# Performance work log

Hardware: AMD Instinct MI355X
Metric: run time of the kernel (lower is better)

## Reference

```python
import jax, jax.numpy as jnp
import numpy as np

N_EMBED = 4096
N_Q_HEADS = 32
N_KV_HEADS = 8
HEAD_DIM = N_EMBED // N_Q_HEADS  # 128
N_GROUPS = N_Q_HEADS // N_KV_HEADS  # 4
ROPE_BASE = 10000.0
BATCH, SEQ = 1, 2048


def setup_inputs() -> dict:
    key = jax.random.key(0)
    ks = jax.random.split(key, 5)
    hidden_state = jax.random.normal(ks[0], (BATCH, SEQ, N_EMBED), dtype=jnp.float32)
    # additive causal mask: 0 on/below diagonal, -inf above (SDPA float-mask semantics)
    causal = jnp.tril(jnp.ones((SEQ, SEQ), dtype=bool))
    attention_mask = jnp.where(causal, 0.0, -jnp.inf).astype(jnp.float32)[None, None]
    position_ids = jnp.arange(SEQ, dtype=jnp.int32)[None, :].repeat(BATCH, axis=0)
    s = 0.02
    Wq = jax.random.normal(ks[1], (N_EMBED, N_EMBED), dtype=jnp.float32) * s
    Wk = jax.random.normal(ks[2], (N_KV_HEADS * HEAD_DIM, N_EMBED), dtype=jnp.float32) * s
    Wv = jax.random.normal(ks[3], (N_KV_HEADS * HEAD_DIM, N_EMBED), dtype=jnp.float32) * s
    Wo = jax.random.normal(ks[4], (N_EMBED, N_EMBED), dtype=jnp.float32) * s
    return {"hidden_state": hidden_state, "attention_mask": attention_mask,
            "position_ids": position_ids, "Wq": Wq, "Wk": Wk, "Wv": Wv, "Wo": Wo}


def _rope_tables(position_ids):
    # mimic torch: inv_freq built in fp16 then used as float
    exponent = (jnp.arange(0, HEAD_DIM, 2, dtype=jnp.float16) / HEAD_DIM)
    inv_freq = (1.0 / (ROPE_BASE ** exponent)).astype(jnp.float32)  # [hd/2]
    m = position_ids.astype(jnp.float32)  # [bs, seq]
    m_theta = m[:, :, None] * inv_freq[None, None, :]  # [bs, seq, hd/2]
    m_theta = jnp.concatenate([m_theta, m_theta], axis=-1)  # [bs, seq, hd]
    return jnp.cos(m_theta), jnp.sin(m_theta)


def _rotate_half(x):
    half = x.shape[-1] // 2
    return jnp.concatenate([-x[..., half:], x[..., :half]], axis=-1)


def reference(hidden_state, attention_mask, position_ids, Wq, Wk, Wv, Wo):
    bs, seq, _ = hidden_state.shape
    q = (hidden_state @ Wq.T).reshape(bs, seq, N_Q_HEADS, HEAD_DIM).transpose(0, 2, 1, 3)
    k = (hidden_state @ Wk.T).reshape(bs, seq, N_KV_HEADS, HEAD_DIM).transpose(0, 2, 1, 3)
    v = (hidden_state @ Wv.T).reshape(bs, seq, N_KV_HEADS, HEAD_DIM).transpose(0, 2, 1, 3)

    cos, sin = _rope_tables(position_ids)
    cos, sin = cos[:, None], sin[:, None]  # broadcast over heads
    q = q * cos + _rotate_half(q) * sin
    k = k * cos + _rotate_half(k) * sin

    # GQA: group query heads per KV head instead of materializing KV copies
    qg = q.reshape(bs, N_KV_HEADS, N_GROUPS, seq, HEAD_DIM)
    scale = 1.0 / jnp.sqrt(jnp.float32(HEAD_DIM))
    scores = jnp.einsum('bhgqd,bhkd->bhgqk', qg, k) * scale + attention_mask[:, :, None]
    probs = jax.nn.softmax(scores, axis=-1)
    attn = jnp.einsum('bhgqk,bhkd->bhgqd', probs, v)  # [bs, kvh, g, seq, hd]
    attn = attn.reshape(bs, N_Q_HEADS, seq, HEAD_DIM).transpose(0, 2, 1, 3).reshape(bs, seq, N_EMBED)
    return attn @ Wo.T
```

## Files before the change

### kernel.cpp

```cpp
#include <hip/hip_runtime.h>
#include <hip/hip_bf16.h>

#define SEQ 2048
#define LDQKV 6144

typedef __attribute__((ext_vector_type(8))) __bf16 bf16x8;
typedef __attribute__((ext_vector_type(4))) __bf16 bf16x4;
typedef __attribute__((ext_vector_type(4))) float f32x4;

__device__ __forceinline__ void gload_lds16(const void* g, void* l) {
  __builtin_amdgcn_global_load_lds((__attribute__((address_space(1))) void*)(g),
                                   (__attribute__((address_space(3))) void*)(l), 16, 0, 0);
}

struct CvtArgs {
  const float* src0; const float* src1; const float* src2; const float* src3; const float* src4;
  __bf16* dst0; __bf16* dst1; __bf16* dst2; __bf16* dst3; __bf16* dst4;
};
__global__ __launch_bounds__(256) void cvt_all(CvtArgs a) {
  int b = blockIdx.x;
  const float* s; __bf16* d; int boff;
  if (b < 4096)       { s = a.src0; d = a.dst0; boff = b; }
  else if (b < 12288) { s = a.src1; d = a.dst1; boff = b - 4096; }
  else if (b < 14336) { s = a.src2; d = a.dst2; boff = b - 12288; }
  else if (b < 16384) { s = a.src3; d = a.dst3; boff = b - 14336; }
  else                { s = a.src4; d = a.dst4; boff = b - 16384; }
  long i = ((long)boff * 256 + threadIdx.x) * 8;
  f32x4 v0 = *(const f32x4*)(s + i);
  f32x4 v1 = *(const f32x4*)(s + i + 4);
  bf16x8 o;
  #pragma unroll
  for (int j = 0; j < 4; ++j) { o[j] = (__bf16)v0[j]; o[j + 4] = (__bf16)v1[j]; }
  *(bf16x8*)(d + i) = o;
}

__global__ __launch_bounds__(256) void rope_tab_k(const int* __restrict__ pos,
                                                  float* __restrict__ tab) {
  int i = blockIdx.x * 256 + threadIdx.x;
  int s = i >> 6, j = i & 63;
  float p = (float)pos[s];
  float pw = powf(10000.0f, (float)j * (1.0f / 64.0f));
  _Float16 ph = (_Float16)pw;
  _Float16 ivh = (_Float16)(1.0f / (float)ph);
  float freq = (float)ivh;
  float th = p * freq;
  tab[i] = cosf(th);
  tab[SEQ * 64 + i] = sinf(th);
}

__global__ __launch_bounds__(256) void rope_apply_k(__bf16* __restrict__ qkv,
                                                    const float* __restrict__ tab) {
  int i = blockIdx.x * 256 + threadIdx.x;
  int dc = i & 7;
  int ht = (i >> 3) % 40;
  int s = i / 320;
  long col = (ht < 32) ? (long)ht * 128 : (long)4096 + (long)(ht - 32) * 128;
  __bf16* p = qkv + (long)s * LDQKV + col + dc * 8;
  bf16x8 lo = *(bf16x8*)p;
  bf16x8 hi = *(bf16x8*)(p + 64);
  const float* tc = tab + (long)s * 64 + dc * 8;
  const float* ts = tc + SEQ * 64;
  bf16x8 lo2, hi2;
  #pragma unroll
  for (int e = 0; e < 8; ++e) {
    float c = tc[e], sn = ts[e];
    float lv = (float)lo[e], hv = (float)hi[e];
    lo2[e] = (__bf16)(lv * c - hv * sn);
    hi2[e] = (__bf16)(hv * c + lv * sn);
  }
  *(bf16x8*)p = lo2;
  *(bf16x8*)(p + 64) = hi2;
}

template<int BN, int BUFS, bool OUT_BF16>
__global__ __launch_bounds__(512, 2) void gemmW(const __bf16* __restrict__ A,
                                                const __bf16* __restrict__ B,
                                                void* __restrict__ C,
                                                int K, int ldc) {
  constexpr int BHR = BN / 2;
  constexpr int NFR = BN / 128;
  constexpr int LB  = BHR / 64;
  constexpr int NA  = (BUFS == 3) ? 2 : 1;
  constexpr int TE  = (128 + BN) * 64;
  extern __shared__ __bf16 lds[];

  const int tid = threadIdx.x;
  const int wave = tid >> 6, lane = tid & 63;
  const int l15 = lane & 15, l4 = lane >> 4;
  const int wm = wave >> 2, wn = wave & 3;

  const int orig = blockIdx.x;
  const int swz = (orig & 7) * 32 + (orig >> 3);
  const int bx = swz & 15, by = swz >> 4;
  const long brow = (long)bx * 128, bcol = (long)by * BN;

  const int rS = tid >> 3;
  const int cS = ((tid & 7) * 8) ^ ((rS & 7) << 3);
  const int NT = K >> 6;

  auto bufp = [&](int b) -> __bf16* { return lds + b * TE; };
  auto stageA = [&](int b, int qm, int t) {
    gload_lds16(A + (brow + qm * 64 + rS) * (long)K + t * 64 + cS,
                bufp(b) + qm * 4096 + wave * 512);
  };
  auto stageB = [&](int b, int qn, int t) {
    #pragma unroll
    for (int i = 0; i < LB; ++i)
      gload_lds16(B + (bcol + qn * BHR + i * 64 + rS) * (long)K + t * 64 + cS,
                  bufp(b) + 8192 + qn * (BHR * 64) + i * 4096 + wave * 512);
  };

  bf16x8 afLo[2][2], afHi[2][2], b0[NFR][2], b1[NFR][2];
  auto readA = [&](bf16x8 (&dst)[2][2], int b, int qm) {
    #pragma unroll
    for (int mi = 0; mi < 2; ++mi) {
      int r = wm * 32 + mi * 16 + l15;
      #pragma unroll
      for (int kf = 0; kf < 2; ++kf) {
        int c = (kf * 32 + l4 * 8) ^ ((r & 7) << 3);
        dst[mi][kf] = *(const bf16x8*)&bufp(b)[qm * 4096 + r * 64 + c];
      }
    }
  };
  auto readB = [&](bf16x8 (&dst)[NFR][2], int b, int qn) {
    #pragma unroll
    for (int ni = 0; ni < NFR; ++ni) {
      int r = wn * (BN / 8) + ni * 16 + l15;
      #pragma unroll
      for (int kf = 0; kf < 2; ++kf) {
        int c = (kf * 32 + l4 * 8) ^ ((r & 7) << 3);
        dst[ni][kf] = *(const bf16x8*)&bufp(b)[8192 + qn * (BHR * 64) + r * 64 + c];
      }
    }
  };

  f32x4 acc[2][2][2][NFR] = {};
  auto mfmaQ = [&](bf16x8 (&af)[2][2], bf16x8 (&bf_)[NFR][2], f32x4 (&ac)[2][NFR]) {
    __builtin_amdgcn_s_setprio(1);
    #pragma unroll
    for (int mi = 0; mi < 2; ++mi)
      #pragma unroll
      for (int ni = 0; ni < NFR; ++ni)
        #pragma unroll
        for (int kf = 0; kf < 2; ++kf)
          ac[mi][ni] = __builtin_amdgcn_mfma_f32_16x16x32_bf16(af[mi][kf], bf_[ni][kf], ac[mi][ni], 0, 0, 0);
    __builtin_amdgcn_s_setprio(0);
  };

  #pragma unroll
  for (int tt = 0; tt < NA; ++tt) {
    stageA(tt % BUFS, 0, tt); stageB(tt % BUFS, 0, tt);
    stageA(tt % BUFS, 1, tt); stageB(tt % BUFS, 1, tt);
  }
  if constexpr (BUFS == 3) asm volatile("s_waitcnt vmcnt(6)" ::: "memory");
  else                     asm volatile("s_waitcnt vmcnt(0)" ::: "memory");
  __builtin_amdgcn_s_barrier();
  __builtin_amdgcn_sched_barrier(0);

  for (int t = 0; t < NT; ++t) {
    const int cur = t % BUFS, pre = (t + NA) % BUFS;
    const bool pf = (t + NA < NT);
    readA(afLo, cur, 0); readB(b0, cur, 0);
    if (pf) { stageA(pre, 0, t + NA); stageB(pre, 0, t + NA); }
    mfmaQ(afLo, b0, acc[0][0]);
    readA(afHi, cur, 1); readB(b1, cur, 1);
    if (pf) { stageA(pre, 1, t + NA); stageB(pre, 1, t + NA); }
    mfmaQ(afHi, b0, acc[1][0]);
    mfmaQ(afHi, b1, acc[1][1]);
    mfmaQ(afLo, b1, acc[0][1]);
    if (t + 1 < NT) {
      __builtin_amdgcn_sched_barrier(0);
      if constexpr (BUFS == 3) {
        if (pf) asm volatile("s_waitcnt vmcnt(6)" ::: "memory");
        else    asm volatile("s_waitcnt vmcnt(0)" ::: "memory");
      } else {
        asm volatile("s_waitcnt vmcnt(0)" ::: "memory");
      }
      __builtin_amdgcn_s_barrier();
      __builtin_amdgcn_sched_barrier(0);
    }
  }

  #pragma unroll
  for (int qm = 0; qm < 2; ++qm)
    #pragma unroll
    for (int qn = 0; qn < 2; ++qn)
      #pragma unroll
      for (int mi = 0; mi < 2; ++mi)
        #pragma unroll
        for (int ni = 0; ni < NFR; ++ni)
          #pragma unroll
          for (int j = 0; j < 4; ++j) {
            long rr = brow + qm * 64 + wm * 32 + mi * 16 + l4 * 4 + j;
            long cc = bcol + qn * BHR + wn * (BN / 8) + ni * 16 + l15;
            float v = acc[qm][qn][mi][ni][j];
            if (OUT_BF16) ((__bf16*)C)[rr * ldc + cc] = (__bf16)v;
            else          ((float*)C)[rr * ldc + cc] = v;
          }
}

__global__ __launch_bounds__(256) void flash_k(const __bf16* __restrict__ qkv,
                                               __bf16* __restrict__ ctx) {
  __shared__ __align__(16) __bf16 Kl[8192];
  __shared__ __align__(16) __bf16 Vt[8192];
  __shared__ __align__(16) __bf16 Pl[4][1024];

  const int bid = blockIdx.x;
  const int h = bid & 31;
  const int qt = 31 - (bid >> 5);
  const int kvh = h >> 2;
  const int q0 = qt * 64;
  const int tid = threadIdx.x, wave = tid >> 6, lane = tid & 63;
  const int l15 = lane & 15, l4 = lane >> 4;
  const int d2 = tid & 63, grp = tid >> 6;

  const __bf16* Qp = qkv + (long)h * 128;
  const __bf16* Kp = qkv + 4096 + (long)kvh * 128;
  const __bf16* Vp = qkv + 5120 + (long)kvh * 128;

  bf16x8 aq[4];
  {
    long qr = q0 + wave * 16 + l15;
    #pragma unroll
    for (int ks = 0; ks < 4; ++ks)
      aq[ks] = *(const bf16x8*)(Qp + qr * LDQKV + ks * 32 + l4 * 8);
  }
  f32x4 accO[8] = {};
  float lsum[4] = {0.f, 0.f, 0.f, 0.f};
  const float cexp = 0.08838834764831845f * 1.4426950408889634f;

  for (int kv0 = 0; kv0 <= q0; kv0 += 64) {
    __syncthreads();
    #pragma unroll
    for (int i = 0; i < 4; ++i) {
      int fo = i * 2048 + wave * 512 + lane * 8;
      int r = fo >> 7, c = fo & 127;
      int cs = c ^ ((r & 7) << 3);
      gload_lds16(Kp + (long)(kv0 + r) * LDQKV + cs, &Kl[i * 2048 + wave * 512]);
    }
    unsigned int vv[2][8];
    #pragma unroll
    for (int rep = 0; rep < 2; ++rep) {
      int cch = grp * 2 + rep;
      #pragma unroll
      for (int i = 0; i < 8; ++i)
        vv[rep][i] = *(const unsigned int*)(Vp + (long)(kv0 + cch * 8 + i) * LDQKV + 2 * d2);
    }
    #pragma unroll
    for (int rep = 0; rep < 2; ++rep) {
      int cch = grp * 2 + rep;
      #pragma unroll
      for (int half = 0; half < 2; ++half) {
        bf16x8 w;
        #pragma unroll
        for (int i = 0; i < 8; ++i)
          w[i] = __builtin_bit_cast(__bf16, (unsigned short)(vv[rep][i] >> (16 * half)));
        int d = 2 * d2 + half;
        *(bf16x8*)&Vt[d * 64 + ((cch * 8) ^ ((d2 & 7) * 8))] = w;
      }
    }
    __syncthreads();

    f32x4 s[4];
    #pragma unroll
    for (int t = 0; t < 4; ++t) s[t] = f32x4{0.f, 0.f, 0.f, 0.f};
    __builtin_amdgcn_s_setprio(1);
    #pragma unroll
    for (int t = 0; t < 4; ++t) {
      int r = t * 16 + l15;
      #pragma unroll
      for (int ks = 0; ks < 4; ++ks) {
        bf16x8 bk = *(const bf16x8*)&Kl[r * 128 + ((ks * 32 + l4 * 8) ^ ((r & 7) << 3))];
        s[t] = __builtin_amdgcn_mfma_f32_16x16x32_bf16(aq[ks], bk, s[t], 0, 0, 0);
      }
    }
    __builtin_amdgcn_s_setprio(0);

    const bool lastStep = (kv0 == q0);
    float pout[4][4];
    #pragma unroll
    for (int t = 0; t < 4; ++t)
      #pragma unroll
      for (int j = 0; j < 4; ++j) {
        float p = exp2f(s[t][j] * cexp);
        if (lastStep) {
          int qg = wave * 16 + l4 * 4 + j;
          int kg = t * 16 + l15;
          if (kg > qg) p = 0.f;
        }
        pout[t][j] = p;
      }
    #pragma unroll
    for (int j = 0; j < 4; ++j)
      lsum[j] += (pout[0][j] + pout[1][j]) + (pout[2][j] + pout[3][j]);

    #pragma unroll
    for (int t = 0; t < 4; ++t)
      #pragma unroll
      for (int j = 0; j < 4; ++j) {
        int r = l4 * 4 + j;
        int c = t * 16 + l15;
        Pl[wave][r * 64 + (c ^ ((r & 7) << 3))] = (__bf16)pout[t][j];
      }
    asm volatile("s_waitcnt lgkmcnt(0)" ::: "memory");
    __builtin_amdgcn_sched_barrier(0);
    bf16x8 ap[2];
    #pragma unroll
    for (int ks2 = 0; ks2 < 2; ++ks2) {
      int c = ks2 * 32 + l4 * 8;
      ap[ks2] = *(const bf16x8*)&Pl[wave][l15 * 64 + (c ^ ((l15 & 7) << 3))];
    }
    __builtin_amdgcn_s_setprio(1);
    #pragma unroll
    for (int dt = 0; dt < 8; ++dt) {
      int d = dt * 16 + l15;
      #pragma unroll
      for (int ks2 = 0; ks2 < 2; ++ks2) {
        int c = (ks2 * 32 + l4 * 8) ^ (((l15 >> 1) & 7) * 8);
        bf16x8 bv = *(const bf16x8*)&Vt[d * 64 + c];
        accO[dt] = __builtin_amdgcn_mfma_f32_16x16x32_bf16(ap[ks2], bv, accO[dt], 0, 0, 0);
      }
    }
    __builtin_amdgcn_s_setprio(0);
  }
  float rls[4];
  #pragma unroll
  for (int j = 0; j < 4; ++j) {
    float ls = lsum[j];
    ls += __shfl_xor(ls, 1, 16);
    ls += __shfl_xor(ls, 2, 16);
    ls += __shfl_xor(ls, 4, 16);
    ls += __shfl_xor(ls, 8, 16);
    rls[j] = 1.f / ls;
  }
  #pragma unroll
  for (int dt = 0; dt < 8; ++dt)
    #pragma unroll
    for (int j = 0; j < 4; ++j) {
      long qr = q0 + wave * 16 + l4 * 4 + j;
      long cc = (long)h * 128 + dt * 16 + l15;
      ctx[qr * 4096 + cc] = (__bf16)(accO[dt][j] * rls[j]);
    }
}

extern "C" void kernel_launch(void* const* d_in, const int* in_sizes, int n_in,
                              void* d_out, int out_size, void* d_ws, size_t ws_size,
                              hipStream_t stream) {
  const float* hs  = (const float*)d_in[0];
  const int*   pos = (const int*)d_in[2];
  const float* Wq  = (const float*)d_in[3];
  const float* Wk  = (const float*)d_in[4];
  const float* Wv  = (const float*)d_in[5];
  const float* Wo  = (const float*)d_in[6];
  char* ws = (char*)d_ws;
  __bf16* hsb  = (__bf16*)(ws + 0L);
  __bf16* wqkv = (__bf16*)(ws + 16777216L);
  __bf16* wob  = (__bf16*)(ws + 67108864L);
  __bf16* qkvb = (__bf16*)(ws + 100663296L);
  float*  tab  = (float*)(ws + 125829120L);
  __bf16* ctx  = (__bf16*)(ws + 126877696L);

  (void)hipFuncSetAttribute(reinterpret_cast<const void*>(&gemmW<384, 2, true>),
                            hipFuncAttributeMaxDynamicSharedMemorySize, 131072);
  (void)hipFuncSetAttribute(reinterpret_cast<const void*>(&gemmW<256, 3, false>),
                            hipFuncAttributeMaxDynamicSharedMemorySize, 147456);

  CvtArgs ca;
  ca.src0 = hs;  ca.dst0 = hsb;
  ca.src1 = Wq;  ca.dst1 = wqkv;
  ca.src2 = Wk;  ca.dst2 = wqkv + 16777216L;
  ca.src3 = Wv;  ca.dst3 = wqkv + 20971520L;
  ca.src4 = Wo;  ca.dst4 = wob;
  cvt_all<<<24576, 256, 0, stream>>>(ca);
  rope_tab_k<<<512, 256, 0, stream>>>(pos, tab);

  gemmW<384, 2, true><<<256, 512, 131072, stream>>>(hsb, wqkv, qkvb, 4096, 6144);

  rope_apply_k<<<2560, 256, 0, stream>>>(qkvb, tab);

  flash_k<<<1024, 256, 0, stream>>>(qkvb, ctx);

  gemmW<256, 3, false><<<256, 512, 147456, stream>>>(ctx, wob, d_out, 4096, 4096);
}
```

Measured before the change: 283.1 us.

## Interleave per-quarter staging with MFMA phases in double-buffered GEMM loop

For the two-buffer GEMM configuration, the main loop is restructured into four phases per k-tile. Each phase issues one quarter-tile global-to-LDS stage for the next tile, runs one MFMA quadrant, then waits on a partial vmcnt and a barrier. The goal is to spread memory traffic across the compute so loads overlap MFMA work, instead of staging everything up front and doing a full vmcnt(0) wait at the end. The cost is more barriers per iteration, and the vmcnt(4) counts only stay correct if each stage call issues the number of loads they assume.

```diff
diff --git a/kernel.cpp b/kernel.cpp
--- a/kernel.cpp
+++ b/kernel.cpp
@@ -147,37 +147,64 @@
     __builtin_amdgcn_s_setprio(0);
   };
 
-  #pragma unroll
-  for (int tt = 0; tt < NA; ++tt) {
-    stageA(tt % BUFS, 0, tt); stageB(tt % BUFS, 0, tt);
-    stageA(tt % BUFS, 1, tt); stageB(tt % BUFS, 1, tt);
-  }
-  if constexpr (BUFS == 3) asm volatile("s_waitcnt vmcnt(6)" ::: "memory");
-  else                     asm volatile("s_waitcnt vmcnt(0)" ::: "memory");
-  __builtin_amdgcn_s_barrier();
-  __builtin_amdgcn_sched_barrier(0);
-
-  for (int t = 0; t < NT; ++t) {
-    const int cur = t % BUFS, pre = (t + NA) % BUFS;
-    const bool pf = (t + NA < NT);
-    readA(afLo, cur, 0); readB(b0, cur, 0);
-    if (pf) { stageA(pre, 0, t + NA); stageB(pre, 0, t + NA); }
-    mfmaQ(afLo, b0, acc[0][0]);
-    readA(afHi, cur, 1); readB(b1, cur, 1);
-    if (pf) { stageA(pre, 1, t + NA); stageB(pre, 1, t + NA); }
-    mfmaQ(afHi, b0, acc[1][0]);
-    mfmaQ(afHi, b1, acc[1][1]);
-    mfmaQ(afLo, b1, acc[0][1]);
-    if (t + 1 < NT) {
-      __builtin_amdgcn_sched_barrier(0);
-      if constexpr (BUFS == 3) {
+  if constexpr (BUFS == 2) {
+    #define VM_WAIT4() asm volatile("s_waitcnt vmcnt(4)" ::: "memory")
+    #define PH_BAR()   do { __builtin_amdgcn_s_barrier(); __builtin_amdgcn_sched_barrier(0); } while (0)
+    stageA(0, 0, 0); stageB(0, 0, 0); stageA(0, 1, 0); stageB(0, 1, 0);
+    VM_WAIT4();
+    PH_BAR();
+    for (int t = 0; t < NT; ++t) {
+      const int buf = t & 1, nb = buf ^ 1;
+      const bool pf = (t + 1 < NT);
+      if (pf) stageA(nb, 0, t + 1);
+      readA(afLo, buf, 0); readB(b0, buf, 0);
+      mfmaQ(afLo, b0, acc[0][0]);
+      VM_WAIT4();
+      PH_BAR();
+      if (pf) stageB(nb, 0, t + 1);
+      readA(afHi, buf, 1);
+      mfmaQ(afHi, b0, acc[1][0]);
+      VM_WAIT4();
+      PH_BAR();
+      if (pf) stageA(nb, 1, t + 1);
+      readB(b1, buf, 1);
+      mfmaQ(afHi, b1, acc[1][1]);
+      PH_BAR();
+      if (pf) stageB(nb, 1, t + 1);
+      mfmaQ(afLo, b1, acc[0][1]);
+      VM_WAIT4();
+      PH_BAR();
+    }
+    #undef VM_WAIT4
+    #undef PH_BAR
+  } else {
+    #pragma unroll
+    for (int tt = 0; tt < NA; ++tt) {
+      stageA(tt % BUFS, 0, tt); stageB(tt % BUFS, 0, tt);
+      stageA(tt % BUFS, 1, tt); stageB(tt % BUFS, 1, tt);
+    }
+    asm volatile("s_waitcnt vmcnt(6)" ::: "memory");
+    __builtin_amdgcn_s_barrier();
+    __builtin_amdgcn_sched_barrier(0);
+
+    for (int t = 0; t < NT; ++t) {
+      const int cur = t % BUFS, pre = (t + NA) % BUFS;
+      const bool pf = (t + NA < NT);
+      readA(afLo, cur, 0); readB(b0, cur, 0);
+      if (pf) { stageA(pre, 0, t + NA); stageB(pre, 0, t + NA); }
+      mfmaQ(afLo, b0, acc[0][0]);
+      readA(afHi, cur, 1); readB(b1, cur, 1);
+      if (pf) { stageA(pre, 1, t + NA); stageB(pre, 1, t + NA); }
+      mfmaQ(afHi, b0, acc[1][0]);
+      mfmaQ(afHi, b1, acc[1][1]);
+      mfmaQ(afLo, b1, acc[0][1]);
+      if (t + 1 < NT) {
+        __builtin_amdgcn_sched_barrier(0);
         if (pf) asm volatile("s_waitcnt vmcnt(6)" ::: "memory");
         else    asm volatile("s_waitcnt vmcnt(0)" ::: "memory");
-      } else {
-        asm volatile("s_waitcnt vmcnt(0)" ::: "memory");
-      }
-      __builtin_amdgcn_s_barrier();
-      __builtin_amdgcn_sched_barrier(0);
+        __builtin_amdgcn_s_barrier();
+        __builtin_amdgcn_sched_barrier(0);
+      }
     }
   }
 
```

Result: slower. 288.8 us (+2.0%).
